# Performance work log

Hardware: AMD Instinct MI355X
Metric: run time of the kernel (lower is better)

## Reference

```python
import jax, jax.numpy as jnp
import numpy as np

CAPACITY_FACTOR = 1.25
NEG_INF = jnp.float32(-1e30)


def setup_inputs() -> dict:
    key = jax.random.key(0)
    k1, k2 = jax.random.split(key)
    hidden_states = jax.random.normal(k1, (4, 4096, 2048), dtype=jnp.float32)
    w_gate = jax.random.normal(k2, (64, 2048), dtype=jnp.float32) * 0.02  # nn.Linear weight [E, D]
    return {"hidden_states": hidden_states, "w_gate": w_gate}


def _switch_route(hidden_states, w_gate):
    B, S, D = hidden_states.shape
    E = w_gate.shape[0]
    N = B * S
    cap = int(N * CAPACITY_FACTOR / E)  # capacity_per_expert

    x = hidden_states.reshape(N, D)
    gate_logits = x @ w_gate.T                       # [N, E]
    gate_probs = jax.nn.softmax(gate_logits, axis=-1)
    expert_weights = jnp.max(gate_probs, axis=-1)    # [N]
    expert_indices = jnp.argmax(gate_probs, axis=-1) # [N] int

    # histogram of routed tokens per expert
    tokens_per_expert = jax.ops.segment_sum(
        jnp.ones((N,), jnp.float32), expert_indices, num_segments=E)

    cap_f = jnp.float32(cap)

    # sequential capacity-enforcement loop over experts (matches torch loop,
    # including the weight-zeroing carried across iterations)
    def step(w, e):
        mask = expert_indices == e
        masked_w = jnp.where(mask, w, NEG_INF)
        _, top_idx = jax.lax.top_k(masked_w, cap)    # top `cap` tokens of this expert
        keep = jnp.zeros((N,), bool).at[top_idx].set(True)
        w_new = w * keep.astype(w.dtype)
        w = jnp.where(tokens_per_expert[e] > cap_f, w_new, w)
        return w, None

    expert_weights, _ = jax.lax.scan(step, expert_weights, jnp.arange(E))

    mean_gate_probs = gate_probs.mean(axis=0)        # [E]
    fraction_per_expert = tokens_per_expert / N
    aux_loss = (fraction_per_expert * mean_gate_probs).sum() * E

    return expert_weights[:, None], expert_indices[:, None], tokens_per_expert, aux_loss


def reference(hidden_states, w_gate):
    return _switch_route(hidden_states, w_gate)
```

## Files before the change

kernel.cpp:

```cpp
#include <hip/hip_runtime.h>
#include <math.h>

#define DD 2048
#define EE 64
#define KQ 32
#define TOKTILE 128
#define KSPLIT 8

__global__ __launch_bounds__(256, 4) void sr_gemm(
    const float* __restrict__ x, const float* __restrict__ wg,
    float* __restrict__ partial, int N)
{
  __shared__ float xs[KQ][TOKTILE];
  __shared__ float wsh[KQ][EE];
  const int ntiles = N / TOKTILE;
  const int tt = blockIdx.x % ntiles;
  const int kc = blockIdx.x / ntiles;
  const int kblk = DD / KSPLIT;
  const int nchunk = kblk / KQ;
  const int k0 = kc * kblk;
  const int t0 = tt * TOKTILE;
  const int tid = threadIdx.x;
  const int ti = tid & 31;
  const int tj = tid >> 5;

  float acc[4][8];
#pragma unroll
  for (int r = 0; r < 4; ++r)
#pragma unroll
    for (int c = 0; c < 8; ++c) acc[r][c] = 0.f;

  const int srowbase = tid >> 3;
  const int c4 = (tid & 7) * 4;
  const int swz = 8 * (tid & 3);

  for (int ch = 0; ch < nchunk; ++ch) {
    const int kb = k0 + ch * KQ;
#pragma unroll
    for (int p = 0; p < 4; ++p) {
      const int row = p * 32 + srowbase;
      const float4 v = *reinterpret_cast<const float4*>(
          &x[(size_t)(t0 + row) * DD + kb + c4]);
      const int srow = row ^ swz;
      xs[c4 + 0][srow] = v.x;
      xs[c4 + 1][srow] = v.y;
      xs[c4 + 2][srow] = v.z;
      xs[c4 + 3][srow] = v.w;
    }
    {
      const int e = tid >> 2;
      const int kq = (tid & 3) * 8;
      const float4 a = *reinterpret_cast<const float4*>(&wg[(size_t)e * DD + kb + kq]);
      const float4 b = *reinterpret_cast<const float4*>(&wg[(size_t)e * DD + kb + kq + 4]);
      wsh[kq + 0][e] = a.x; wsh[kq + 1][e] = a.y; wsh[kq + 2][e] = a.z; wsh[kq + 3][e] = a.w;
      wsh[kq + 4][e] = b.x; wsh[kq + 5][e] = b.y; wsh[kq + 6][e] = b.z; wsh[kq + 7][e] = b.w;
    }
    __syncthreads();
#pragma unroll 8
    for (int k = 0; k < KQ; ++k) {
      const int sk = 8 * ((k >> 2) & 3);
      float xv[4], wv[8];
      *reinterpret_cast<float4*>(&xv[0]) =
          *reinterpret_cast<const float4*>(&xs[k][(4 * ti) ^ sk]);
      *reinterpret_cast<float4*>(&wv[0]) = *reinterpret_cast<const float4*>(&wsh[k][8 * tj]);
      *reinterpret_cast<float4*>(&wv[4]) = *reinterpret_cast<const float4*>(&wsh[k][8 * tj + 4]);
#pragma unroll
      for (int r = 0; r < 4; ++r)
#pragma unroll
        for (int c = 0; c < 8; ++c) acc[r][c] = fmaf(xv[r], wv[c], acc[r][c]);
    }
    __syncthreads();
  }
#pragma unroll
  for (int c = 0; c < 8; ++c) {
    const int e = 8 * tj + c;
    const float4 v = make_float4(acc[0][c], acc[1][c], acc[2][c], acc[3][c]);
    *reinterpret_cast<float4*>(&partial[((size_t)kc * EE + e) * N + t0 + 4 * ti]) = v;
  }
}

__global__ __launch_bounds__(256) void sr_reduce(
    const float* __restrict__ partial, float* __restrict__ logits,
    int* __restrict__ counts, int N)
{
  if (blockIdx.x == 0 && threadIdx.x < EE) counts[threadIdx.x] = 0;
  const int i4 = blockIdx.x * 256 + threadIdx.x;
  const size_t base = (size_t)i4 * 4;
  if (base >= (size_t)EE * N) return;
  const size_t cs = (size_t)EE * N;
  double s0 = 0.0, s1 = 0.0, s2 = 0.0, s3 = 0.0;
#pragma unroll
  for (int c = 0; c < KSPLIT; ++c) {
    const float4 v = *reinterpret_cast<const float4*>(&partial[c * cs + base]);
    s0 += (double)v.x; s1 += (double)v.y; s2 += (double)v.z; s3 += (double)v.w;
  }
  *reinterpret_cast<float4*>(&logits[base]) =
      make_float4((float)s0, (float)s1, (float)s2, (float)s3);
}

__global__ __launch_bounds__(256) void sr_softmax(
    const float* __restrict__ logits, float* __restrict__ dout,
    float* __restrict__ ws_w, int* __restrict__ ws_idx,
    int* __restrict__ counts, float* __restrict__ probsum, int N)
{
  __shared__ float lp[128][EE + 1];
  __shared__ float psq[4][EE];
  const int tid = threadIdx.x;
  const int t0 = blockIdx.x * 128;
  if (tid < 128) {
    const int t = t0 + tid;
    float l[EE];
    float maxv = -3.0e38f;
    int arg = 0;
#pragma unroll
    for (int e = 0; e < EE; ++e) {
      l[e] = logits[(size_t)e * N + t];
      if (l[e] > maxv) { maxv = l[e]; arg = e; }
    }
    float s = 0.f;
#pragma unroll
    for (int e = 0; e < EE; ++e) {
      const float ex = __expf(l[e] - maxv);
      lp[tid][e] = ex;
      s += ex;
    }
    const float inv = 1.0f / s;
    const float w = inv;
#pragma unroll
    for (int e = 0; e < EE; ++e) lp[tid][e] *= inv;
    dout[t] = w;
    dout[N + t] = (float)arg;
    ws_w[t] = w;
    ws_idx[t] = arg;
    atomicAdd(&counts[arg], 1);
  }
  __syncthreads();
  const int e = tid & 63, q = tid >> 6;
  float ps = 0.f;
  for (int r = 0; r < 32; ++r) ps += lp[q * 32 + r][e];
  psq[q][e] = ps;
  __syncthreads();
  if (tid < 64) {
    const float tot = ((psq[0][tid] + psq[1][tid]) + psq[2][tid]) + psq[3][tid];
    probsum[(size_t)blockIdx.x * EE + tid] = tot;
  }
}

__device__ __forceinline__ int sr_bsum(int c, int red[][16], int pc, int tid) {
#pragma unroll
  for (int off = 32; off > 0; off >>= 1) c += __shfl_down(c, off, 64);
  if ((tid & 63) == 0) red[pc & 1][tid >> 6] = c;
  __syncthreads();
  int s = 0;
#pragma unroll
  for (int i = 0; i < 16; ++i) s += red[pc & 1][i];
  return s;
}

__global__ __launch_bounds__(1024) void sr_finish(
    const float* __restrict__ probsum, const int* __restrict__ counts,
    const float* __restrict__ ws_w, const int* __restrict__ ws_idx,
    float* __restrict__ dout, int N, int nblocks, int cap)
{
  __shared__ double dseg[16][EE];
  __shared__ double mean_s[EE];
  __shared__ int cnt_s[EE];
  __shared__ int hdr[2];
  __shared__ int red[2][16];
  const int tid = threadIdx.x;
  const int PER = N / 1024;

  float wv[16];
  int iv[16];
#pragma unroll
  for (int r = 0; r < 16; ++r) {
    float w = 0.f; int ix = -1;
    if (r < PER) {
      const int i = tid + r * 1024;
      w = ws_w[i];
      ix = ws_idx[i];
    }
    wv[r] = w; iv[r] = ix;
  }

  {
    const int e = tid & 63, seg = tid >> 6;
    const int per = nblocks / 16;
    double ps = 0.0;
    for (int b = seg * per; b < (seg + 1) * per; ++b)
      ps += (double)probsum[(size_t)b * EE + e];
    dseg[seg][e] = ps;
  }
  __syncthreads();
  if (tid < 64) {
    double tot = 0.0;
#pragma unroll
    for (int s2 = 0; s2 < 16; ++s2) tot += dseg[s2][tid];
    const int cnt = counts[tid];
    dout[2 * N + tid] = (float)cnt;
    mean_s[tid] = tot / (double)N;
    cnt_s[tid] = cnt;
  }
  __syncthreads();
  if (tid == 0) {
    double aux = 0.0;
    int nover = 0, e1 = -1;
    for (int i = 0; i < EE; ++i) {
      aux += ((double)cnt_s[i] / (double)N) * mean_s[i];
      if (cnt_s[i] > cap) { if (nover == 0) e1 = i; ++nover; }
    }
    dout[2 * N + EE] = (float)(aux * (double)EE);
    hdr[0] = (nover >= 2) ? 2 : nover;
    hdr[1] = e1;
  }
  __syncthreads();
  const int mode = hdr[0];

  if (mode == 0) return;
  if (mode == 2) {
#pragma unroll
    for (int r = 0; r < 16; ++r)
      if (r < PER) dout[tid + r * 1024] = 0.f;
    return;
  }

  const int e1 = hdr[1];
  unsigned mb[16];
#pragma unroll
  for (int r = 0; r < 16; ++r)
    mb[r] = (iv[r] == e1) ? __float_as_uint(wv[r]) : 0u;

  int pc = 0;
  unsigned lo = 0x3C000000u, hi = 0x3F800000u;
  while (hi - lo > 1u) {
    const unsigned mid = lo + ((hi - lo) >> 1);
    int c = 0;
#pragma unroll
    for (int r = 0; r < 16; ++r) c += (mb[r] >= mid);
    const int tot = sr_bsum(c, red, pc++, tid);
    if (tot >= cap) lo = mid; else hi = mid;
  }
  int cge = 0, cgt = 0;
#pragma unroll
  for (int r = 0; r < 16; ++r) {
    cge += (mb[r] >= lo);
    cgt += (mb[r] > lo);
  }
  const int tot_ge = sr_bsum(cge, red, pc++, tid);
  const int tot_gt = sr_bsum(cgt, red, pc++, tid);
  const int quota = cap - tot_gt;
  int idx_thr = N - 1;
  if (tot_ge - tot_gt > quota) {
    int l2 = -1, h2 = N - 1;
    while (h2 - l2 > 1) {
      const int mid = (l2 + h2) >> 1;
      int c = 0;
#pragma unroll
      for (int r = 0; r < 16; ++r) {
        const int i = tid + r * 1024;
        c += (mb[r] == lo && i <= mid) ? 1 : 0;
      }
      const int tot = sr_bsum(c, red, pc++, tid);
      if (tot >= quota) h2 = mid; else l2 = mid;
    }
    idx_thr = h2;
  }

#pragma unroll
  for (int r = 0; r < 16; ++r) {
    if (r < PER) {
      const int i = tid + r * 1024;
      const bool keep = (mb[r] > lo) || (mb[r] == lo && i <= idx_thr);
      dout[i] = keep ? wv[r] : 0.f;
    }
  }
}

extern "C" void kernel_launch(void* const* d_in, const int* in_sizes, int n_in,
                              void* d_out, int out_size, void* d_ws, size_t ws_size,
                              hipStream_t stream)
{
  const float* x = (const float*)d_in[0];
  const float* wg = (const float*)d_in[1];
  const int N = in_sizes[0] / DD;
  float* dout = (float*)d_out;
  float* wsf = (float*)d_ws;

  float* ws_w = wsf;
  int* ws_idx = (int*)(wsf + N);
  int* counts = (int*)(wsf + 2 * (size_t)N);
  float* probsum = wsf + 2 * (size_t)N + EE;
  const int nblocks_sm = N / 128;
  float* logits = wsf + 2 * (size_t)N + EE + (size_t)nblocks_sm * EE;
  float* partial = logits + (size_t)EE * N;
  const int cap = (int)((double)N * 1.25 / (double)EE);

  sr_gemm<<<(N / TOKTILE) * KSPLIT, 256, 0, stream>>>(x, wg, partial, N);
  sr_reduce<<<(EE * N / 4 + 255) / 256, 256, 0, stream>>>(partial, logits, counts, N);
  sr_softmax<<<N / 128, 256, 0, stream>>>(logits, dout, ws_w, ws_idx, counts, probsum, N);
  sr_finish<<<1, 1024, 0, stream>>>(probsum, counts, ws_w, ws_idx, dout, N, nblocks_sm, cap);
}
```

Measured before the change: 133.2 us.

## Add 16-way split-K gate GEMM with 256-token tiles when workspace allows

Adds a second gate GEMM kernel that uses 256-token tiles with an 8x8 per-thread register tile and splits K sixteen ways, plus a templated reduce that sums 16 partials. The larger tile lowers how often x and weights are reread per FMA, and the wider K split keeps the block count high. The cost is twice as much partial-sum traffic through the reduce kernel and higher register pressure. The old 8-way path remains as a fallback when the workspace is too small.

```diff
diff --git a/kernel.cpp b/kernel.cpp
--- a/kernel.cpp
+++ b/kernel.cpp
@@ -5,9 +5,8 @@
 #define EE 64
 #define KQ 32
 #define TOKTILE 128
-#define KSPLIT 8
-
-__global__ __launch_bounds__(256, 4) void sr_gemm(
+
+__global__ __launch_bounds__(256, 4) void sr_gemm8(
     const float* __restrict__ x, const float* __restrict__ wg,
     float* __restrict__ partial, int N)
 {
@@ -16,7 +15,7 @@
   const int ntiles = N / TOKTILE;
   const int tt = blockIdx.x % ntiles;
   const int kc = blockIdx.x / ntiles;
-  const int kblk = DD / KSPLIT;
+  const int kblk = DD / 8;
   const int nchunk = kblk / KQ;
   const int k0 = kc * kblk;
   const int t0 = tt * TOKTILE;
@@ -79,7 +78,92 @@
   }
 }
 
-__global__ __launch_bounds__(256) void sr_reduce(
+#define TOK16 256
+#define KQ2 16
+__global__ __launch_bounds__(256, 4) void sr_gemm16(
+    const float* __restrict__ x, const float* __restrict__ wg,
+    float* __restrict__ partial, int N)
+{
+  __shared__ float xs[KQ2][TOK16];
+  __shared__ float wsh[KQ2][EE];
+  const int ntiles = N / TOK16;
+  const int tt = blockIdx.x % ntiles;
+  const int kc = blockIdx.x / ntiles;
+  const int kblk = DD / 16;
+  const int nchunk = kblk / KQ2;
+  const int k0 = kc * kblk;
+  const int t0 = tt * TOK16;
+  const int tid = threadIdx.x;
+  const int ti = tid & 31;
+  const int tj = tid >> 5;
+
+  float acc[8][8];
+#pragma unroll
+  for (int r = 0; r < 8; ++r)
+#pragma unroll
+    for (int c = 0; c < 8; ++c) acc[r][c] = 0.f;
+
+  const int srowb = tid >> 2;
+  const int c4s = (tid & 3) * 4;
+  const int swz = 8 * (tid & 3);
+  const int we = tid >> 2;
+  const int wk4 = (tid & 3) * 4;
+
+  for (int ch = 0; ch < nchunk; ++ch) {
+    const int kb = k0 + ch * KQ2;
+#pragma unroll
+    for (int p = 0; p < 4; ++p) {
+      const int row = p * 64 + srowb;
+      const float4 v = *reinterpret_cast<const float4*>(
+          &x[(size_t)(t0 + row) * DD + kb + c4s]);
+      const int srow = row ^ swz;
+      xs[c4s + 0][srow] = v.x;
+      xs[c4s + 1][srow] = v.y;
+      xs[c4s + 2][srow] = v.z;
+      xs[c4s + 3][srow] = v.w;
+    }
+    {
+      const float4 a = *reinterpret_cast<const float4*>(
+          &wg[(size_t)we * DD + kb + wk4]);
+      wsh[wk4 + 0][we] = a.x;
+      wsh[wk4 + 1][we] = a.y;
+      wsh[wk4 + 2][we] = a.z;
+      wsh[wk4 + 3][we] = a.w;
+    }
+    __syncthreads();
+#pragma unroll
+    for (int k = 0; k < KQ2; ++k) {
+      const int sk = 8 * ((k >> 2) & 3);
+      const int xb = (8 * ti) ^ sk;
+      float xv[8], wv[8];
+      *reinterpret_cast<float4*>(&xv[0]) =
+          *reinterpret_cast<const float4*>(&xs[k][xb]);
+      *reinterpret_cast<float4*>(&xv[4]) =
+          *reinterpret_cast<const float4*>(&xs[k][xb + 4]);
+      *reinterpret_cast<float4*>(&wv[0]) =
+          *reinterpret_cast<const float4*>(&wsh[k][8 * tj]);
+      *reinterpret_cast<float4*>(&wv[4]) =
+          *reinterpret_cast<const float4*>(&wsh[k][8 * tj + 4]);
+#pragma unroll
+      for (int r = 0; r < 8; ++r)
+#pragma unroll
+        for (int c = 0; c < 8; ++c) acc[r][c] = fmaf(xv[r], wv[c], acc[r][c]);
+    }
+    __syncthreads();
+  }
+#pragma unroll
+  for (int c = 0; c < 8; ++c) {
+    const int e = 8 * tj + c;
+    const size_t base = ((size_t)kc * EE + e) * N + t0 + 8 * ti;
+    *reinterpret_cast<float4*>(&partial[base]) =
+        make_float4(acc[0][c], acc[1][c], acc[2][c], acc[3][c]);
+    *reinterpret_cast<float4*>(&partial[base + 4]) =
+        make_float4(acc[4][c], acc[5][c], acc[6][c], acc[7][c]);
+  }
+}
+
+template <int KS>
+__global__ __launch_bounds__(256) void sr_reduceT(
     const float* __restrict__ partial, float* __restrict__ logits,
     int* __restrict__ counts, int N)
 {
@@ -90,7 +174,7 @@
   const size_t cs = (size_t)EE * N;
   double s0 = 0.0, s1 = 0.0, s2 = 0.0, s3 = 0.0;
 #pragma unroll
-  for (int c = 0; c < KSPLIT; ++c) {
+  for (int c = 0; c < KS; ++c) {
     const float4 v = *reinterpret_cast<const float4*>(&partial[c * cs + base]);
     s0 += (double)v.x; s1 += (double)v.y; s2 += (double)v.z; s3 += (double)v.w;
   }
@@ -293,10 +377,19 @@
   const int nblocks_sm = N / 128;
   float* logits = wsf + 2 * (size_t)N + EE + (size_t)nblocks_sm * EE;
   float* partial = logits + (size_t)EE * N;
+  const size_t base_floats = 2 * (size_t)N + EE + (size_t)nblocks_sm * EE + (size_t)EE * N;
   const int cap = (int)((double)N * 1.25 / (double)EE);
 
-  sr_gemm<<<(N / TOKTILE) * KSPLIT, 256, 0, stream>>>(x, wg, partial, N);
-  sr_reduce<<<(EE * N / 4 + 255) / 256, 256, 0, stream>>>(partial, logits, counts, N);
+  const bool use16 =
+      (base_floats + (size_t)16 * EE * (size_t)N) * sizeof(float) <= ws_size;
+
+  if (use16) {
+    sr_gemm16<<<(N / TOK16) * 16, 256, 0, stream>>>(x, wg, partial, N);
+    sr_reduceT<16><<<(EE * N / 4 + 255) / 256, 256, 0, stream>>>(partial, logits, counts, N);
+  } else {
+    sr_gemm8<<<(N / TOKTILE) * 8, 256, 0, stream>>>(x, wg, partial, N);
+    sr_reduceT<8><<<(EE * N / 4 + 255) / 256, 256, 0, stream>>>(partial, logits, counts, N);
+  }
   sr_softmax<<<N / 128, 256, 0, stream>>>(logits, dout, ws_w, ws_idx, counts, probsum, N);
   sr_finish<<<1, 1024, 0, stream>>>(probsum, counts, ws_w, ws_idx, dout, N, nblocks_sm, cap);
 }
```

After: 143.5 us. 1.08x slower.
